# Kernel optimization log

Measured on AMD Instinct MI355X. Metric: run time of the kernel, lower is better.

The kernel has to match this reference:

```python
import jax, jax.numpy as jnp
import numpy as np

B, S, DIM, EXTRA, NK, NH, NL = 16, 256, 41, 1, 128, 4, 3
ND = DIM + EXTRA  # 42 channels after appending the Time2Vec extra channel


def _lin(key, fin, fout):
    kw, kb = jax.random.split(key)
    w = jax.random.normal(kw, (fin, fout), jnp.float32) / np.float32(np.sqrt(fin))
    b = jax.random.normal(kb, (fout,), jnp.float32) * 0.01
    return w, b


def _stack(key, fin, fout):
    ws, bs = zip(*[_lin(k, fin, fout) for k in jax.random.split(key, NL)])
    return jnp.stack(ws), jnp.stack(bs)


def setup_inputs():
    key = jax.random.key(0)
    ks = jax.random.split(key, 32)
    inp = {}
    inp['context_x'] = jnp.sort(jax.random.uniform(ks[0], (B, S), jnp.float32), axis=1)
    inp['value'] = jax.random.normal(ks[1], (B, S, DIM), jnp.float32)
    mask = (jax.random.uniform(ks[2], (B, S, DIM)) < 0.23).astype(jnp.float32)
    inp['mask'] = mask
    inp['target_value'] = jax.random.normal(ks[3], (B, S, DIM), jnp.float32)
    inp['target_mask'] = mask * (jax.random.uniform(ks[4], (B, S, DIM)) < 0.3).astype(jnp.float32)
    inp['t2v_w0'] = jax.random.normal(ks[5], (1,), jnp.float32)
    inp['t2v_b0'] = jax.random.normal(ks[6], (1,), jnp.float32)
    inp['edge_w'], inp['edge_b'] = _lin(ks[7], 2, NK)
    inp['chan_w'], inp['chan_b'] = _lin(ks[8], ND, NK)
    inp['time_w'], inp['time_b'] = _lin(ks[9], 1, NK)
    base = 10
    for pre, dk in (('ct', 2 * NK), ('tc', 2 * NK), ('ca', NK)):
        inp[pre + '_wq'], inp[pre + '_bq'] = _stack(ks[base], NK, NK); base += 1
        inp[pre + '_wk'], inp[pre + '_bk'] = _stack(ks[base], dk, NK); base += 1
        inp[pre + '_wv'], inp[pre + '_bv'] = _stack(ks[base], dk, NK); base += 1
        inp[pre + '_wo'], inp[pre + '_bo'] = _stack(ks[base], NK, NK); base += 1
    inp['en_w'], inp['en_b'] = _stack(ks[base], 3 * NK, NK); base += 1
    inp['out_w'], inp['out_b'] = _lin(ks[base], 3 * NK, 1)
    return inp


def _mab2(Q, K, wq, bq, wk, bk, wv, bv, wo, bo, mask):
    # GraFITi MAB2: fc_q/fc_k/fc_v -> dim_out, multihead attn, O = Q + A@V, then O += relu(fc_o(O))
    q = Q @ wq + bq
    k = K @ wk + bk
    v = K @ wv + bv
    b, nq, d = q.shape
    dh = d // NH
    qh = q.reshape(b, nq, NH, dh)
    kh = k.reshape(b, -1, NH, dh)
    vh = v.reshape(b, -1, NH, dh)
    att = jnp.einsum('bqhd,bkhd->bhqk', qh, kh) / np.float32(np.sqrt(d))
    if mask is not None:
        att = jnp.where(mask[:, None] == 0, jnp.float32(-1e10), att)
    A = jax.nn.softmax(att, axis=-1)
    o = (qh + jnp.einsum('bhqk,bkhd->bqhd', A, vh)).reshape(b, nq, d)
    return o + jax.nn.relu(o @ wo + bo)


def _forward(context_x, value, mask, target_value, target_mask, t2v_w0, t2v_b0,
             edge_w, edge_b, chan_w, chan_b, time_w, time_b,
             ct_wq, ct_bq, ct_wk, ct_bk, ct_wv, ct_bv, ct_wo, ct_bo,
             tc_wq, tc_bq, tc_wk, tc_bk, tc_wv, tc_bv, tc_wo, tc_bo,
             en_w, en_b,
             ca_wq, ca_bq, ca_wk, ca_bk, ca_wv, ca_bv, ca_wo, ca_bo,
             out_w, out_b):
    te = (t2v_w0 * context_x + t2v_b0)[:, :, None]  # Time2Vec linear channel [B,S,1]
    value_f = jnp.concatenate([value, te], -1)  # [B,S,ND]
    mask_f = jnp.concatenate([mask, jnp.ones((B, S, EXTRA), jnp.float32)], -1)
    tval_f = jnp.concatenate([target_value, te], -1)
    tmask_f = jnp.concatenate([target_mask, jnp.zeros((B, S, EXTRA), jnp.float32)], -1)
    # ragged compaction: observed entries first, zero-padded to the batch max count
    full_len = int(np.asarray(jnp.max(jnp.sum(mask_f, axis=(1, 2)))))
    order = jnp.argsort(-mask_f.reshape(B, -1), axis=1, stable=True)[:, :full_len]
    take = lambda x: jnp.take_along_axis(x.reshape(B, -1), order, axis=1)
    mk_ = take(mask_f)  # [B,L]: ones then zero padding
    U_val = take(value_f) * mk_
    target_U_ = take(tval_f) * mk_
    target_mask_ = take(tmask_f) * mk_
    mki = mk_.astype(jnp.int32)
    T_inds_ = take(jnp.broadcast_to(jnp.arange(S, dtype=jnp.int32)[None, :, None], (B, S, ND))) * mki
    C_inds_ = take(jnp.broadcast_to(jnp.arange(ND, dtype=jnp.int32)[None, None, :], (B, S, ND))) * mki
    C_mask = (C_inds_[:, None, :] == jnp.arange(ND)[None, :, None]).astype(jnp.float32) * mk_[:, None, :]
    T_mask = (T_inds_[:, None, :] == jnp.arange(S)[None, :, None]).astype(jnp.float32) * mk_[:, None, :]
    U_ind = 1.0 - mk_ + target_mask_
    U = jax.nn.relu(jnp.stack([U_val, U_ind], -1) @ edge_w + edge_b) * mk_[:, :, None]  # [B,L,NK]
    T_ = jnp.sin(context_x[:, :, None] @ time_w + time_b)  # [B,S,NK]
    # one_hot(arange(ND)) @ chan_w == chan_w
    C_ = jnp.broadcast_to(jax.nn.relu(chan_w + chan_b)[None], (B, ND, NK))
    gT = lambda x, idx: jnp.take_along_axis(x, jnp.broadcast_to(idx[:, :, None], (B, full_len, NK)), axis=1)
    for i in range(NL):
        k_t = gT(T_, T_inds_)
        C2 = _mab2(C_, jnp.concatenate([k_t, U], -1), ct_wq[i], ct_bq[i], ct_wk[i], ct_bk[i], ct_wv[i], ct_bv[i], ct_wo[i], ct_bo[i], C_mask)
        k_c = gT(C_, C_inds_)
        T2 = _mab2(T_, jnp.concatenate([k_c, U], -1), tc_wq[i], tc_bq[i], tc_wk[i], tc_bk[i], tc_wv[i], tc_bv[i], tc_wo[i], tc_bo[i], T_mask)
        U = jax.nn.relu(U + jnp.concatenate([U, k_t, k_c], -1) @ en_w[i] + en_b[i]) * mk_[:, :, None]
        C_ = _mab2(C2, C2, ca_wq[i], ca_bq[i], ca_wk[i], ca_bk[i], ca_wv[i], ca_bv[i], ca_wo[i], ca_bo[i], None)
        T_ = T2
    k_t = gT(T_, T_inds_)
    k_c = gT(C_, C_inds_)
    output = jnp.concatenate([U, k_t, k_c], -1) @ out_w + out_b  # [B,L,1]
    return output, target_U_, target_mask_


def reference(context_x, value, mask, target_value, target_mask, t2v_w0, t2v_b0, edge_w, edge_b, chan_w, chan_b, time_w, time_b, ct_wq, ct_bq, ct_wk, ct_bk, ct_wv, ct_bv, ct_wo, ct_bo, tc_wq, tc_bq, tc_wk, tc_bk, tc_wv, tc_bv, tc_wo, tc_bo, en_w, en_b, ca_wq, ca_bq, ca_wk, ca_bk, ca_wv, ca_bv, ca_wo, ca_bo, out_w, out_b):
    return _forward(context_x, value, mask, target_value, target_mask, t2v_w0, t2v_b0, edge_w, edge_b, chan_w, chan_b, time_w, time_b, ct_wq, ct_bq, ct_wk, ct_bk, ct_wv, ct_bv, ct_wo, ct_bo, tc_wq, tc_bq, tc_wk, tc_bk, tc_wv, tc_bv, tc_wo, tc_bo, en_w, en_b, ca_wq, ca_bq, ca_wk, ca_bk, ca_wv, ca_bv, ca_wo, ca_bo, out_w, out_b)
```

## Files before the change

### kernel.cpp

```cpp
#include <hip/hip_runtime.h>
#include <math.h>

#define NB   16
#define SS   256
#define DIMV 41
#define NDV  42
#define NKD  128
#define NHD  4
#define DH   32
#define NLAY 3
#define TOT  (SS*NDV)
#define NCH  42

typedef __attribute__((ext_vector_type(8))) short short8;
typedef __attribute__((ext_vector_type(4))) float floatx4;

__device__ __forceinline__ short f2bf(float x) {
    unsigned u = __float_as_uint(x);
    u += 0x7fff + ((u >> 16) & 1);
    return (short)(u >> 16);
}
__device__ __forceinline__ float bfs2f(short s) {
    return __uint_as_float(((unsigned)(unsigned short)s) << 16);
}
__device__ __forceinline__ float bf2f(unsigned s) {
    return __uint_as_float(s << 16);
}

struct Seg { const short* ptr; const int* ind; int ns; };

__device__ __forceinline__ const short* seg_row(const Seg s, int gm, int Lb) {
    if (s.ind) {
        int b = gm / Lb;
        int id = s.ind[gm]; if (id < 0) id = 0;
        return s.ptr + ((size_t)b * s.ns + (size_t)id) * NKD;
    }
    return s.ptr + (size_t)gm * NKD;
}


__device__ __forceinline__ void compactA_body(int bx, const float* __restrict__ maskp,
                                              int* __restrict__ chunkcnt)
{
    const int b = bx / NCH, ch = bx % NCH;
    const int tid = threadIdx.x;
    const int idx = ch * 256 + tid;
    const int s = idx / NDV, c = idx % NDV;
    float m = (c < DIMV) ? maskp[((size_t)b*SS + s)*DIMV + c] : 1.0f;
    int x = (m != 0.0f) ? 1 : 0;
    #pragma unroll
    for (int off = 32; off; off >>= 1) x += __shfl_down(x, off);
    __shared__ int ws4[4];
    if ((tid & 63) == 0) ws4[tid >> 6] = x;
    __syncthreads();
    if (tid == 0) chunkcnt[bx] = ws4[0] + ws4[1] + ws4[2] + ws4[3];
}

__device__ __forceinline__ void zero_body(int bx, int* __restrict__ lo_t,
                                          int* __restrict__ hi_t)
{
    int i = bx*256 + threadIdx.x;
    if (i < NB*SS) { lo_t[i] = 0; hi_t[i] = 0; }
}

__device__ __forceinline__ void initT_body(int bx, const float* __restrict__ cx,
                                           const float* __restrict__ tw,
                                           const float* __restrict__ tb,
                                           short* __restrict__ T)
{
    int i = bx * 256 + threadIdx.x;
    if (i >= NB*SS*16) return;
    int row = i >> 4;
    int k = (i & 15) << 3;
    float t = cx[row];
    short8 r;
    #pragma unroll
    for (int j = 0; j < 8; j++) r[j] = f2bf(sinf(t*tw[k+j] + tb[k+j]));
    *(short8*)(T + (size_t)row*NKD + k) = r;
}

__device__ __forceinline__ void initC_body(int bx, const float* __restrict__ cw,
                                           const float* __restrict__ cb,
                                           short* __restrict__ C)
{
    int i = bx * 256 + threadIdx.x;
    if (i >= NB*NDV*16) return;
    int row = i >> 4;
    int c = row % NDV;
    int k = (i & 15) << 3;
    short8 r;
    #pragma unroll
    for (int j = 0; j < 8; j++) r[j] = f2bf(fmaxf(cw[(size_t)c*NKD + k+j] + cb[k+j], 0.f));
    *(short8*)(C + (size_t)row*NKD + k) = r;
}

template<int Kg>
__device__ __forceinline__ void prep1(const float* __restrict__ src,
                                      short* __restrict__ dst, int rel)
{
    const int per = Kg*128;
    int i = rel / per; int r2 = rel - i*per;
    int n = r2 / Kg;   int k = r2 - n*Kg;
    dst[rel] = f2bf(src[(size_t)i*per + (size_t)k*128 + n]);
}

#define W_TOTAL 933888
__device__ __forceinline__ void prepw_body(int bx,
    const float* ctq, const float* ctk, const float* ctv, const float* cto,
    const float* tcq, const float* tck, const float* tcv, const float* tco,
    const float* caq, const float* cak, const float* cav, const float* cao,
    const float* enw, short* __restrict__ arena)
{
    int idx = bx*256 + threadIdx.x;
    if (idx >= W_TOTAL) return;
    if      (idx < 49152 ) prep1<128>(ctq, arena + 0,      idx - 0);
    else if (idx < 147456) prep1<256>(ctk, arena + 49152,  idx - 49152);
    else if (idx < 245760) prep1<256>(ctv, arena + 147456, idx - 147456);
    else if (idx < 294912) prep1<128>(cto, arena + 245760, idx - 245760);
    else if (idx < 344064) prep1<128>(tcq, arena + 294912, idx - 294912);
    else if (idx < 442368) prep1<256>(tck, arena + 344064, idx - 344064);
    else if (idx < 540672) prep1<256>(tcv, arena + 442368, idx - 442368);
    else if (idx < 589824) prep1<128>(tco, arena + 540672, idx - 540672);
    else if (idx < 638976) prep1<128>(caq, arena + 589824, idx - 589824);
    else if (idx < 688128) prep1<128>(cak, arena + 638976, idx - 638976);
    else if (idx < 737280) prep1<128>(cav, arena + 688128, idx - 688128);
    else if (idx < 786432) prep1<128>(cao, arena + 737280, idx - 737280);
    else                   prep1<384>(enw, arena + 786432, idx - 786432);
}

__device__ __forceinline__ void trange_body(int bx, const int* __restrict__ tind,
                                            int* __restrict__ lo_t,
                                            int* __restrict__ hi_t, int L)
{
    int p = bx*256 + threadIdx.x;
    if (p >= NB*L) return;
    int b = p / L, l = p - b*L;
    int t = tind[p];
    if (t < 0) return;
    int tp = (l > 0) ? tind[p-1] : -999;
    int tn = (l+1 < L) ? tind[p+1] : -999;
    if (tp != t) lo_t[b*SS + t] = l;
    if (tn != t) hi_t[b*SS + t] = l+1;
}

__device__ __forceinline__ void cperm_body(int b, const int* __restrict__ cind,
                                           int* __restrict__ invp,
                                           int* __restrict__ clo,
                                           int* __restrict__ chi, int L)
{
    __shared__ int hist[NDV];
    __shared__ int base[NDV];
    __shared__ int padc, cntsh;
    const int tid = threadIdx.x;
    if (tid < NDV) hist[tid] = 0;
    if (tid == 0) padc = 0;
    __syncthreads();
    for (int l = tid; l < L; l += 256) {
        int c = cind[(size_t)b*L + l];
        if (c >= 0) atomicAdd(&hist[c], 1);
    }
    __syncthreads();
    if (tid == 0) {
        int run = 0;
        for (int c = 0; c < NDV; c++) {
            base[c] = run; clo[b*NDV + c] = run;
            run += hist[c]; chi[b*NDV + c] = run;
        }
        cntsh = run;
    }
    __syncthreads();
    if (tid < NDV) hist[tid] = 0;
    __syncthreads();
    const int cnt = cntsh;
    for (int l = tid; l < L; l += 256) {
        int c = cind[(size_t)b*L + l];
        int pos;
        if (c >= 0) pos = base[c] + atomicAdd(&hist[c], 1);
        else        pos = cnt + atomicAdd(&padc, 1);
        invp[(size_t)b*L + l] = b*L + pos;
    }
}

__device__ __forceinline__ void initU_body(int bx, const float* __restrict__ uval,
                                           const float* __restrict__ uind,
                                           const float* __restrict__ mkb,
                                           const float* __restrict__ ew,
                                           const float* __restrict__ eb,
                                           short* __restrict__ U, int BL)
{
    int i = bx * 256 + threadIdx.x;
    if (i >= BL*16) return;
    int row = i >> 4;
    int k = (i & 15) << 3;
    float uv = uval[row], ui = uind[row], m = mkb[row];
    short8 r;
    #pragma unroll
    for (int j = 0; j < 8; j++)
        r[j] = f2bf(fmaxf(uv*ew[k+j] + ui*ew[NKD+k+j] + eb[k+j], 0.f) * m);
    *(short8*)(U + (size_t)row*NKD + k) = r;
}

template<int NSEG, int MODE>
__device__ __forceinline__ void mgemm_body(char* smem, int bx,
           Seg s0, Seg s1, Seg s2, const short* __restrict__ Wt,
           const float* __restrict__ bias, short* __restrict__ D,
           int M, int Lb, const float* __restrict__ mkp)
{
    short (*As)[40] = (short (*)[40])smem;
    short (*Bs)[40] = (short (*)[40])(smem + 10240);
    const int bm = bx * 128;
    const int tid = threadIdx.x;
    const int wv = tid >> 6;
    const int lane = tid & 63;
    const int quad = lane >> 4;
    const int l16 = lane & 15;
    const int K = NSEG * 128;
    floatx4 acc[2][8];
    #pragma unroll
    for (int i = 0; i < 2; i++)
        #pragma unroll
        for (int j = 0; j < 8; j++) acc[i][j] = (floatx4){0.f,0.f,0.f,0.f};

    const int arow = tid >> 1;
    const int acol = (tid & 1) * 16;
    int gmc = bm + arow; if (gmc > M-1) gmc = M-1;
    const short* rowp0 = seg_row(s0, gmc, Lb);
    const short* rowp1 = (NSEG > 1) ? seg_row(s1, gmc, Lb) : nullptr;
    const short* rowp2 = (NSEG > 2) ? seg_row(s2, gmc, Lb) : nullptr;

    for (int k0 = 0; k0 < K; k0 += 32) {
        {
            const short* rp;
            if (NSEG == 1) rp = rowp0;
            else if (NSEG == 2) rp = (k0 < 128) ? rowp0 : rowp1;
            else rp = (k0 < 128) ? rowp0 : ((k0 < 256) ? rowp1 : rowp2);
            const int ks = k0 & 127;
            const short* src = rp + ks + acol;
            *(short8*)&As[arow][acol]   = *(const short8*)(src);
            *(short8*)&As[arow][acol+8] = *(const short8*)(src+8);
        }
        {
            const short* src = Wt + (size_t)arow*K + k0 + acol;
            *(short8*)&Bs[arow][acol]   = *(const short8*)(src);
            *(short8*)&Bs[arow][acol+8] = *(const short8*)(src+8);
        }
        __syncthreads();
        short8 af0 = *(short8*)&As[wv*32 + l16][quad*8];
        short8 af1 = *(short8*)&As[wv*32 + 16 + l16][quad*8];
        #pragma unroll
        for (int nf = 0; nf < 8; nf++) {
            short8 bf = *(short8*)&Bs[nf*16 + l16][quad*8];
            acc[0][nf] = __builtin_amdgcn_mfma_f32_16x16x32_bf16(af0, bf, acc[0][nf], 0, 0, 0);
            acc[1][nf] = __builtin_amdgcn_mfma_f32_16x16x32_bf16(af1, bf, acc[1][nf], 0, 0, 0);
        }
        __syncthreads();
    }
    #pragma unroll
    for (int mf = 0; mf < 2; mf++) {
        #pragma unroll
        for (int r = 0; r < 4; r++) {
            int gm = bm + wv*32 + mf*16 + quad*4 + r;
            if (gm < M) {
                float mk = (MODE == 3) ? mkp[gm] : 0.f;
                const short* res = (MODE == 2 || MODE == 3) ? seg_row(s0, gm, Lb) : nullptr;
                #pragma unroll
                for (int nf = 0; nf < 8; nf++) {
                    int gn = nf*16 + l16;
                    float val = acc[mf][nf][r] + bias[gn];
                    if (MODE == 2) val = bfs2f(res[gn]) + fmaxf(val, 0.f);
                    else if (MODE == 3) val = fmaxf(bfs2f(res[gn]) + val, 0.f) * mk;
                    D[(size_t)gm*NKD + gn] = f2bf(val);
                }
            }
        }
    }
}

template<int NSEG>
__device__ __forceinline__ void mgemm_kv_body(char* smem, int bx,
              Seg s0, Seg s1,
              const short* __restrict__ Wk, const float* __restrict__ bk,
              const short* __restrict__ Wv, const float* __restrict__ bv,
              unsigned* __restrict__ KV, int M, int Lb, const int* __restrict__ rmap)
{
    short (*As)[40] = (short (*)[40])smem;
    short (*Bk_)[40] = (short (*)[40])(smem + 5120);
    short (*Bv_)[40] = (short (*)[40])(smem + 15360);
    const int bm = bx * 64;
    const int tid = threadIdx.x;
    const int wv = tid >> 6;
    const int lane = tid & 63;
    const int quad = lane >> 4;
    const int l16 = lane & 15;
    const int K = NSEG * 128;
    floatx4 acck[8], accv[8];
    #pragma unroll
    for (int j = 0; j < 8; j++) {
        acck[j] = (floatx4){0.f,0.f,0.f,0.f};
        accv[j] = (floatx4){0.f,0.f,0.f,0.f};
    }

    const int arow = tid >> 2;
    const int acol = (tid & 3) * 8;
    const int brow = tid >> 1;
    const int bcol = (tid & 1) * 16;
    int gmc = bm + arow; if (gmc > M-1) gmc = M-1;
    const short* rowp0 = seg_row(s0, gmc, Lb);
    const short* rowp1 = (NSEG > 1) ? seg_row(s1, gmc, Lb) : nullptr;

    for (int k0 = 0; k0 < K; k0 += 32) {
        {
            const short* rp = (NSEG == 1) ? rowp0 : ((k0 < 128) ? rowp0 : rowp1);
            const int ks = k0 & 127;
            *(short8*)&As[arow][acol] = *(const short8*)(rp + ks + acol);
        }
        {
            const short* sk = Wk + (size_t)brow*K + k0 + bcol;
            *(short8*)&Bk_[brow][bcol]   = *(const short8*)(sk);
            *(short8*)&Bk_[brow][bcol+8] = *(const short8*)(sk+8);
            const short* sv = Wv + (size_t)brow*K + k0 + bcol;
            *(short8*)&Bv_[brow][bcol]   = *(const short8*)(sv);
            *(short8*)&Bv_[brow][bcol+8] = *(const short8*)(sv+8);
        }
        __syncthreads();
        short8 af = *(short8*)&As[wv*16 + l16][quad*8];
        #pragma unroll
        for (int nf = 0; nf < 8; nf++) {
            short8 bfk = *(short8*)&Bk_[nf*16 + l16][quad*8];
            acck[nf] = __builtin_amdgcn_mfma_f32_16x16x32_bf16(af, bfk, acck[nf], 0, 0, 0);
            short8 bfv = *(short8*)&Bv_[nf*16 + l16][quad*8];
            accv[nf] = __builtin_amdgcn_mfma_f32_16x16x32_bf16(af, bfv, accv[nf], 0, 0, 0);
        }
        __syncthreads();
    }
    #pragma unroll
    for (int r = 0; r < 4; r++) {
        int gm = bm + wv*16 + quad*4 + r;
        if (gm < M) {
            int orow = rmap ? rmap[gm] : gm;
            #pragma unroll
            for (int nf = 0; nf < 8; nf++) {
                int gn = nf*16 + l16;
                float kf = acck[nf][r] + bk[gn];
                float vf = accv[nf][r] + bv[gn];
                unsigned pk = (unsigned)(unsigned short)f2bf(kf)
                            | ((unsigned)(unsigned short)f2bf(vf) << 16);
                KV[(size_t)orow*NKD + gn] = pk;
            }
        }
    }
}

__device__ __forceinline__ void octca_body(char* smem, int bx,
    const short* __restrict__ oC,
    const short* __restrict__ wo, const float* __restrict__ bo,
    const short* __restrict__ wq, const float* __restrict__ bq,
    const short* __restrict__ wk, const float* __restrict__ bk,
    const short* __restrict__ wv, const float* __restrict__ bv,
    short* __restrict__ qC, unsigned* __restrict__ KV, int M)
{
    short (*C2t)[136] = (short (*)[136])smem;
    short (*Bs)[40]   = (short (*)[40])(smem + 17408);
    short (*As)[40]   = (short (*)[40])(smem + 27648);
    const int bm = bx * 64;
    const int tid = threadIdx.x;
    const int wv_ = tid >> 6;
    const int lane = tid & 63;
    const int quad = lane >> 4;
    const int l16 = lane & 15;
    const int arow = tid >> 2;
    const int acol = (tid & 3) * 8;
    const int brow = tid >> 1;
    const int bcol = (tid & 1) * 16;
    int gmc = bm + arow; if (gmc > M-1) gmc = M-1;
    const short* rowp = oC + (size_t)gmc * NKD;

    floatx4 acc[8];
    #pragma unroll
    for (int j = 0; j < 8; j++) acc[j] = (floatx4){0.f,0.f,0.f,0.f};
    for (int k0 = 0; k0 < 128; k0 += 32) {
        *(short8*)&As[arow][acol] = *(const short8*)(rowp + k0 + acol);
        const short* sw = wo + (size_t)brow*128 + k0 + bcol;
        *(short8*)&Bs[brow][bcol]   = *(const short8*)(sw);
        *(short8*)&Bs[brow][bcol+8] = *(const short8*)(sw+8);
        __syncthreads();
        short8 af = *(short8*)&As[wv_*16 + l16][quad*8];
        #pragma unroll
        for (int nf = 0; nf < 8; nf++) {
            short8 bf = *(short8*)&Bs[nf*16 + l16][quad*8];
            acc[nf] = __builtin_amdgcn_mfma_f32_16x16x32_bf16(af, bf, acc[nf], 0, 0, 0);
        }
        __syncthreads();
    }
    #pragma unroll
    for (int r = 0; r < 4; r++) {
        int lrow = wv_*16 + quad*4 + r;
        int gm = bm + lrow; int gmr = (gm > M-1) ? (M-1) : gm;
        const short* res = oC + (size_t)gmr*NKD;
        #pragma unroll
        for (int nf = 0; nf < 8; nf++) {
            int gn = nf*16 + l16;
            float val = acc[nf][r] + bo[gn];
            val = bfs2f(res[gn]) + fmaxf(val, 0.f);
            C2t[lrow][gn] = f2bf(val);
        }
    }
    __syncthreads();

    floatx4 acck[8];
    for (int proj = 0; proj < 3; proj++) {
        const short* W = (proj == 0) ? wq : ((proj == 1) ? wk : wv);
        floatx4 a2[8];
        #pragma unroll
        for (int j = 0; j < 8; j++) a2[j] = (floatx4){0.f,0.f,0.f,0.f};
        for (int k0 = 0; k0 < 128; k0 += 32) {
            const short* sw = W + (size_t)brow*128 + k0 + bcol;
            *(short8*)&Bs[brow][bcol]   = *(const short8*)(sw);
            *(short8*)&Bs[brow][bcol+8] = *(const short8*)(sw+8);
            __syncthreads();
            short8 af = *(short8*)&C2t[wv_*16 + l16][k0 + quad*8];
            #pragma unroll
            for (int nf = 0; nf < 8; nf++) {
                short8 bf = *(short8*)&Bs[nf*16 + l16][quad*8];
                a2[nf] = __builtin_amdgcn_mfma_f32_16x16x32_bf16(af, bf, a2[nf], 0, 0, 0);
            }
            __syncthreads();
        }
        if (proj == 0) {
            #pragma unroll
            for (int r = 0; r < 4; r++) {
                int gm = bm + wv_*16 + quad*4 + r;
                if (gm < M) {
                    #pragma unroll
                    for (int nf = 0; nf < 8; nf++) {
                        int gn = nf*16 + l16;
                        qC[(size_t)gm*NKD + gn] = f2bf(a2[nf][r] + bq[gn]);
                    }
                }
            }
        } else if (proj == 1) {
            #pragma unroll
            for (int j = 0; j < 8; j++) acck[j] = a2[j];
        } else {
            #pragma unroll
            for (int r = 0; r < 4; r++) {
                int gm = bm + wv_*16 + quad*4 + r;
                if (gm < M) {
                    #pragma unroll
                    for (int nf = 0; nf < 8; nf++) {
                        int gn = nf*16 + l16;
                        float kf = acck[nf][r] + bk[gn];
                        float vf = a2[nf][r] + bv[gn];
                        KV[(size_t)gm*NKD + gn] =
                            (unsigned)(unsigned short)f2bf(kf)
                          | ((unsigned)(unsigned short)f2bf(vf) << 16);
                    }
                }
            }
        }
    }
}

template<int SPLIT>
__device__ __forceinline__ void sattn_body(int bx,
                  const short* __restrict__ q, const unsigned* __restrict__ kvb,
                  short* __restrict__ o, int nq, int nkv,
                  const int* __restrict__ lo_arr, const int* __restrict__ hi_arr)
{
    __shared__ float sm_m[4], sm_s[4], sm_a[4][DH];
    const int wvid = threadIdx.x >> 6;
    int gtask = bx * 4 + wvid;
    int task = gtask / SPLIT;
    int part = gtask % SPLIT;
    if (task >= NB * nq * NHD) return;
    const int h = task & 3;
    const int bq = task >> 2;
    const int qi = bq % nq;
    const int b = bq / nq;
    const int lane = threadIdx.x & 63;
    const int d = lane & 31;
    const int half = lane >> 5;
    int lo = lo_arr ? lo_arr[b*nq + qi] : 0;
    int hi = hi_arr ? hi_arr[b*nq + qi] : nkv;
    if (SPLIT == 2) {
        int mid = lo + ((hi - lo + 1) >> 1);
        if (part == 0) hi = mid; else lo = mid;
    }
    const float scale = 0.088388347648318447f;

    const float qv = bfs2f(q[((size_t)(b*nq + qi))*NKD + h*DH + d]);
    const unsigned* kb = kvb + (size_t)b*nkv*NKD + h*DH + d;

    float m = -INFINITY, ssum = 0.f, acc = 0.f;
    for (int l0 = lo; l0 < hi; l0 += 8) {
        unsigned ur[4];
        #pragma unroll
        for (int j = 0; j < 4; j++) {
            int l = l0 + 2*j + half;
            bool ok = (l < hi);
            ur[j] = ok ? kb[(size_t)l*NKD] : 0u;
        }
        #pragma unroll
        for (int j = 0; j < 4; j++) {
            int l = l0 + 2*j + half;
            float kr = bf2f(ur[j] & 0xffffu);
            float vr = bf2f(ur[j] >> 16);
            float partial = qv * kr;
            #pragma unroll
            for (int off = 16; off; off >>= 1) partial += __shfl_xor(partial, off);
            float s = partial * scale;
            if (l < hi) {
                float mn = fmaxf(m, s);
                float corr = __expf(m - mn);
                float p = __expf(s - mn);
                ssum = ssum * corr + p;
                acc  = acc  * corr + p * vr;
                m = mn;
            }
        }
    }
    float mo = __shfl_xor(m, 32);
    float M = fmaxf(m, mo);
    float corr = (m > -1e30f) ? __expf(m - M) : 0.f;
    ssum *= corr; acc *= corr;
    ssum += __shfl_xor(ssum, 32);
    acc  += __shfl_xor(acc, 32);

    if (SPLIT == 1) {
        if (half == 0) {
            float res = (ssum > 0.f) ? acc / ssum : 0.f;
            o[((size_t)(b*nq + qi))*NKD + h*DH + d] = f2bf(qv + res);
        }
    } else {
        if (lane == 0) { sm_m[wvid] = M; sm_s[wvid] = ssum; }
        if (lane < DH) sm_a[wvid][lane] = acc;
        __syncthreads();
        if (part == 0 && lane < DH) {
            float m2 = sm_m[wvid+1], s2 = sm_s[wvid+1], a2 = sm_a[wvid+1][lane];
            float M2 = fmaxf(M, m2);
            float c1 = (M  > -1e30f) ? __expf(M  - M2) : 0.f;
            float c2 = (m2 > -1e30f) ? __expf(m2 - M2) : 0.f;
            float S = ssum * c1 + s2 * c2;
            float A = acc  * c1 + a2 * c2;
            float res = (S > 0.f) ? A / S : 0.f;
            float qv2 = bfs2f(q[((size_t)(b*nq + qi))*NKD + h*DH + lane]);
            o[((size_t)(b*nq + qi))*NKD + h*DH + lane] = f2bf(qv2 + res);
        }
    }
}


__global__ __launch_bounds__(256)
void k_pre1(const float* maskp, int* chunkcnt, int* lo_t, int* hi_t,
            const float* cx, const float* tw, const float* tb, short* T,
            const float* cw, const float* cb, short* C,
            const float* ctq, const float* ctk, const float* ctv, const float* cto,
            const float* tcq, const float* tck, const float* tcv, const float* tco,
            const float* caq, const float* cak, const float* cav, const float* cao,
            const float* enw, short* arena)
{
    int bx = blockIdx.x;
    if (bx < NB*NCH)            compactA_body(bx, maskp, chunkcnt);
    else if (bx < NB*NCH + 16)  zero_body(bx - NB*NCH, lo_t, hi_t);
    else if (bx < NB*NCH + 16 + 256) initT_body(bx - NB*NCH - 16, cx, tw, tb, T);
    else if (bx < NB*NCH + 16 + 256 + 42) initC_body(bx - NB*NCH - 16 - 256, cw, cb, C);
    else prepw_body(bx - NB*NCH - 16 - 256 - 42,
                    ctq, ctk, ctv, cto, tcq, tck, tcv, tco,
                    caq, cak, cav, cao, enw, arena);
}

__global__ __launch_bounds__(256)
void k_compactC(const float* __restrict__ cx, const float* __restrict__ value,
              const float* __restrict__ maskp, const float* __restrict__ tval,
              const float* __restrict__ tmaskp, const float* __restrict__ w0p,
              const float* __restrict__ b0p,
              const int* __restrict__ chunkcnt, int L,
              int* __restrict__ tind, int* __restrict__ cind,
              float* __restrict__ mkb, float* __restrict__ uval,
              float* __restrict__ uind,
              float* __restrict__ outTU, float* __restrict__ outTM)
{
    const int blk = blockIdx.x;
    const int b = blk / NCH, ch = blk % NCH;
    const int tid = threadIdx.x, lane = tid & 63, wv = tid >> 6;
    const int idx = ch * 256 + tid;
    const int s = idx / NDV, c = idx % NDV;
    float mval = (c < DIMV) ? maskp[((size_t)b*SS + s)*DIMV + c] : 1.0f;
    int m = (mval != 0.0f) ? 1 : 0;
    int x = m;
    #pragma unroll
    for (int off = 1; off < 64; off <<= 1) {
        int y = __shfl_up(x, off);
        if (lane >= off) x += y;
    }
    __shared__ int wsum[4];
    __shared__ int s_off, s_cnt;
    if (lane == 63) wsum[wv] = x;
    if (tid < 64) {
        int v2 = (tid < NCH) ? chunkcnt[b*NCH + tid] : 0;
        int x2 = v2;
        #pragma unroll
        for (int off = 1; off < 64; off <<= 1) {
            int y2 = __shfl_up(x2, off);
            if (tid >= off) x2 += y2;
        }
        if (tid == ch) s_off = x2 - v2;
        if (tid == 63) s_cnt = x2;
    }
    __syncthreads();
    int wbase = 0;
    for (int w = 0; w < wv; w++) wbase += wsum[w];
    const int excl = x - m + wbase;
    const int vbefore = s_off + excl;
    const int cnt = s_cnt;
    const int pos = m ? vbefore : (cnt + (idx - vbefore));
    if (pos < L) {
        const float w0 = w0p[0], b0 = b0p[0];
        float te = w0 * cx[(size_t)b*SS + s] + b0;
        float vf, tvf, tmf;
        if (c < DIMV) {
            size_t o = ((size_t)b*SS + s)*DIMV + c;
            vf = value[o]; tvf = tval[o]; tmf = tmaskp[o];
        } else { vf = te; tvf = te; tmf = 0.0f; }
        size_t p = (size_t)b*L + pos;
        if (m) {
            tind[p] = s; cind[p] = c; mkb[p] = 1.0f;
            uval[p] = vf; uind[p] = tmf;
            outTU[p] = tvf; outTM[p] = tmf;
        } else {
            tind[p] = -1; cind[p] = -1; mkb[p] = 0.0f;
            uval[p] = 0.0f; uind[p] = 1.0f;
            outTU[p] = 0.0f; outTM[p] = 0.0f;
        }
    }
}

__global__ __launch_bounds__(256)
void k_pre4(const int* tind, int* lo_t, int* hi_t, int L, int gTr,
            const int* cind, int* invp, int* clo, int* chi,
            const float* uval, const float* uind, const float* mkb,
            const float* ew, const float* eb, short* U, int BL)
{
    int bx = blockIdx.x;
    if (bx < gTr) trange_body(bx, tind, lo_t, hi_t, L);
    else if (bx < gTr + NB) cperm_body(bx - gTr, cind, invp, clo, chi, L);
    else initU_body(bx - gTr - NB, uval, uind, mkb, ew, eb, U, BL);
}

__global__ __launch_bounds__(256)
void k_phase1(int g0, int g1, int g2,
              const short* T1, const int* tind, const short* U,
              const short* wkct, const float* bkct, const short* wvct, const float* bvct,
              unsigned* KVct, const int* invp,
              const short* C1, const short* wqct, const float* bqct, short* qC,
              const int* cind,
              const short* wktc, const float* bktc, const short* wvtc, const float* bvtc,
              unsigned* KVtc,
              const short* wqtc, const float* bqtc, short* qT,
              int BL, int L)
{
    __shared__ __align__(16) char smem[25600];
    int bx = blockIdx.x;
    if (bx < g0) {
        mgemm_kv_body<2>(smem, bx, Seg{T1,tind,SS}, Seg{U,nullptr,0},
            wkct, bkct, wvct, bvct, KVct, BL, L, invp);
    } else if (bx < g0+g1) {
        mgemm_body<1,0>(smem, bx-g0, Seg{C1,nullptr,0}, Seg{nullptr,nullptr,0},
            Seg{nullptr,nullptr,0}, wqct, bqct, qC, NB*NDV, 1, nullptr);
    } else if (bx < g0+g1+g2) {
        mgemm_kv_body<2>(smem, bx-g0-g1, Seg{C1,cind,NDV}, Seg{U,nullptr,0},
            wktc, bktc, wvtc, bvtc, KVtc, BL, L, nullptr);
    } else {
        mgemm_body<1,0>(smem, bx-g0-g1-g2, Seg{T1,nullptr,0}, Seg{nullptr,nullptr,0},
            Seg{nullptr,nullptr,0}, wqtc, bqtc, qT, NB*SS, 1, nullptr);
    }
}

__global__ __launch_bounds__(256)
void k_phase2(int g0, const short* qC, const unsigned* KVct, short* oC,
              const int* clo, const int* chi, int L,
              const short* qT, const unsigned* KVtc, short* oT,
              const int* lo_t, const int* hi_t)
{
    int bx = blockIdx.x;
    if (bx < g0) sattn_body<2>(bx, qC, KVct, oC, NDV, L, clo, chi);
    else         sattn_body<1>(bx-g0, qT, KVtc, oT, SS, L, lo_t, hi_t);
}

__global__ __launch_bounds__(256)
void k_phase3(int g0, int g1,
              const short* oC, const short* woct, const float* boct,
              const short* wq_ca, const float* bq_ca,
              const short* wk_ca, const float* bk_ca,
              const short* wv_ca, const float* bv_ca,
              short* qC, unsigned* kvCa,
              const short* oT, const short* wotc, const float* botc, short* T2b,
              const short* U, const short* T1, const int* tind,
              const short* C1, const int* cind,
              const short* wen, const float* ben, short* Unew, const float* mkb,
              int BL, int L)
{
    __shared__ __align__(16) char smem[32768];
    int bx = blockIdx.x;
    if (bx < g0)
        octca_body(smem, bx, oC, woct, boct, wq_ca, bq_ca, wk_ca, bk_ca,
                   wv_ca, bv_ca, qC, kvCa, NB*NDV);
    else if (bx < g0+g1)
        mgemm_body<1,2>(smem, bx-g0, Seg{oT,nullptr,0}, Seg{nullptr,nullptr,0},
            Seg{nullptr,nullptr,0}, wotc, botc, T2b, NB*SS, 1, nullptr);
    else
        mgemm_body<3,3>(smem, bx-g0-g1, Seg{U,nullptr,0}, Seg{T1,tind,SS},
            Seg{C1,cind,NDV}, wen, ben, Unew, BL, L, mkb);
}

__global__ __launch_bounds__(256)
void k_ca_fused(const short* __restrict__ qC, const unsigned* __restrict__ kv,
                const short* __restrict__ wo, const float* __restrict__ bo,
                short* __restrict__ C1)
{
    __shared__ __align__(16) short os[NKD];
    const int row = blockIdx.x;
    const int b = row / NDV;
    const int tid = threadIdx.x;
    const int h = tid >> 6;
    const int lane = tid & 63;
    const int d = lane & 31;
    const int half = lane >> 5;
    const float scale = 0.088388347648318447f;

    const float qv = bfs2f(qC[(size_t)row*NKD + h*DH + d]);
    const unsigned* kb = kv + (size_t)b*NDV*NKD + h*DH + d;

    float m = -INFINITY, ssum = 0.f, acc = 0.f;
    for (int l0 = 0; l0 < NDV; l0 += 2) {
        int l = l0 + half;
        unsigned ur = kb[(size_t)l*NKD];
        float kr = bf2f(ur & 0xffffu);
        float vr = bf2f(ur >> 16);
        float partial = qv * kr;
        #pragma unroll
        for (int off = 16; off; off >>= 1) partial += __shfl_xor(partial, off);
        float s = partial * scale;
        float mn = fmaxf(m, s);
        float corr = __expf(m - mn);
        float p = __expf(s - mn);
        ssum = ssum * corr + p;
        acc  = acc  * corr + p * vr;
        m = mn;
    }
    float mo = __shfl_xor(m, 32);
    float M = fmaxf(m, mo);
    float corr = (m > -1e30f) ? __expf(m - M) : 0.f;
    ssum *= corr; acc *= corr;
    ssum += __shfl_xor(ssum, 32);
    acc  += __shfl_xor(acc, 32);
    if (half == 0) {
        float res = (ssum > 0.f) ? acc / ssum : 0.f;
        os[h*DH + d] = f2bf(qv + res);
    }
    __syncthreads();

    const int n = tid >> 1;
    const int ks = (tid & 1) * 64;
    float a = 0.f;
    const short* wrow = wo + (size_t)n*NKD + ks;
    #pragma unroll
    for (int kk = 0; kk < 64; kk += 8) {
        short8 o8 = *(short8*)&os[ks + kk];
        short8 w8 = *(const short8*)(wrow + kk);
        #pragma unroll
        for (int j = 0; j < 8; j++) a += bfs2f(o8[j]) * bfs2f(w8[j]);
    }
    a += __shfl_xor(a, 1);
    if ((tid & 1) == 0) {
        float val = a + bo[n];
        val = bfs2f(os[n]) + fmaxf(val, 0.f);
        C1[(size_t)row*NKD + n] = f2bf(val);
    }
}

__global__ __launch_bounds__(256)
void k_out(const short* __restrict__ U, const short* __restrict__ T1,
           const short* __restrict__ C1, const int* __restrict__ tind,
           const int* __restrict__ cind, const float* __restrict__ ow,
           const float* __restrict__ obp, float* __restrict__ out,
           int BL, int L)
{
    int row = blockIdx.x * 4 + (threadIdx.x >> 6);
    int lane = threadIdx.x & 63;
    if (row >= BL) return;
    int b = row / L;
    int ti = tind[row]; if (ti < 0) ti = 0;
    int ci = cind[row]; if (ci < 0) ci = 0;
    const short* u = U + (size_t)row*NKD;
    const short* a = T1 + ((size_t)(b*SS + ti))*NKD;
    const short* c = C1 + ((size_t)(b*NDV + ci))*NKD;
    float s = bfs2f(u[lane])*ow[lane]     + bfs2f(u[lane+64])*ow[lane+64]
            + bfs2f(a[lane])*ow[128+lane] + bfs2f(a[lane+64])*ow[192+lane]
            + bfs2f(c[lane])*ow[256+lane] + bfs2f(c[lane+64])*ow[320+lane];
    #pragma unroll
    for (int off = 32; off; off >>= 1) s += __shfl_down(s, off);
    if (lane == 0) out[row] = s + obp[0];
}

extern "C" void kernel_launch(void* const* d_in, const int* in_sizes, int n_in,
                              void* d_out, int out_size, void* d_ws, size_t ws_size,
                              hipStream_t stream)
{
    const float* cx     = (const float*)d_in[0];
    const float* value  = (const float*)d_in[1];
    const float* maskp  = (const float*)d_in[2];
    const float* tval   = (const float*)d_in[3];
    const float* tmaskp = (const float*)d_in[4];
    const float* w0     = (const float*)d_in[5];
    const float* b0     = (const float*)d_in[6];
    const float* edge_w = (const float*)d_in[7];
    const float* edge_b = (const float*)d_in[8];
    const float* chan_w = (const float*)d_in[9];
    const float* chan_b = (const float*)d_in[10];
    const float* time_w = (const float*)d_in[11];
    const float* time_b = (const float*)d_in[12];
    const float* ct_wq = (const float*)d_in[13];
    const float* ct_bq = (const float*)d_in[14];
    const float* ct_wk = (const float*)d_in[15];
    const float* ct_bk = (const float*)d_in[16];
    const float* ct_wv = (const float*)d_in[17];
    const float* ct_bv = (const float*)d_in[18];
    const float* ct_wo = (const float*)d_in[19];
    const float* ct_bo = (const float*)d_in[20];
    const float* tc_wq = (const float*)d_in[21];
    const float* tc_bq = (const float*)d_in[22];
    const float* tc_wk = (const float*)d_in[23];
    const float* tc_bk = (const float*)d_in[24];
    const float* tc_wv = (const float*)d_in[25];
    const float* tc_bv = (const float*)d_in[26];
    const float* tc_wo = (const float*)d_in[27];
    const float* tc_bo = (const float*)d_in[28];
    const float* ca_wq = (const float*)d_in[29];
    const float* ca_bq = (const float*)d_in[30];
    const float* ca_wk = (const float*)d_in[31];
    const float* ca_bk = (const float*)d_in[32];
    const float* ca_wv = (const float*)d_in[33];
    const float* ca_bv = (const float*)d_in[34];
    const float* ca_wo = (const float*)d_in[35];
    const float* ca_bo = (const float*)d_in[36];
    const float* en_w  = (const float*)d_in[37];
    const float* en_b  = (const float*)d_in[38];
    const float* out_w = (const float*)d_in[39];
    const float* out_b = (const float*)d_in[40];

    const int BL = out_size / 3;
    const int L  = BL / NB;

    char* p = (char*)d_ws;
    auto alloc = [&](size_t n) { char* r = p; p += (n + 255) & ~(size_t)255; return r; };
    int*      tind   = (int*)  alloc((size_t)BL*4);
    int*      cind   = (int*)  alloc((size_t)BL*4);
    float*    mkb    = (float*)alloc((size_t)BL*4);
    float*    uval   = (float*)alloc((size_t)BL*4);
    float*    uind   = (float*)alloc((size_t)BL*4);
    int*      lo_t   = (int*)  alloc((size_t)NB*SS*4);
    int*      hi_t   = (int*)  alloc((size_t)NB*SS*4);
    int*      clo    = (int*)  alloc((size_t)NB*NDV*4);
    int*      chi    = (int*)  alloc((size_t)NB*NDV*4);
    int*      invp   = (int*)  alloc((size_t)BL*4);
    int*      chunkc = (int*)  alloc((size_t)NB*NCH*4);
    short*    waren  = (short*)alloc((size_t)W_TOTAL*2);
    short*    U    = (short*)alloc((size_t)BL*NKD*2);
    short*    Unew = (short*)alloc((size_t)BL*NKD*2);
    unsigned* KVct = (unsigned*)alloc((size_t)BL*NKD*4);
    unsigned* KVtc = (unsigned*)alloc((size_t)BL*NKD*4);
    unsigned* kvCa = (unsigned*)alloc((size_t)NB*NDV*NKD*4);
    short*    T1   = (short*)alloc((size_t)NB*SS*NKD*2);
    short*    T2b  = (short*)alloc((size_t)NB*SS*NKD*2);
    short*    qT   = (short*)alloc((size_t)NB*SS*NKD*2);
    short*    oT   = (short*)alloc((size_t)NB*SS*NKD*2);
    short*    C1   = (short*)alloc((size_t)NB*NDV*NKD*2);
    short*    qC   = (short*)alloc((size_t)NB*NDV*NKD*2);
    short*    oC   = (short*)alloc((size_t)NB*NDV*NKD*2);

    float* outMain = (float*)d_out;
    float* outTU = outMain + BL;
    float* outTM = outMain + 2*BL;

    const size_t OCTQ=0, OCTK=49152, OCTV=147456, OCTO=245760;
    const size_t OTCQ=294912, OTCK=344064, OTCV=442368, OTCO=540672;
    const size_t OCAQ=589824, OCAK=638976, OCAV=688128, OCAO=737280, OEN=786432;

    k_pre1<<<NB*NCH + 16 + 256 + 42 + W_TOTAL/256, 256, 0, stream>>>(
        maskp, chunkc, lo_t, hi_t, cx, time_w, time_b, T1, chan_w, chan_b, C1,
        ct_wq, ct_wk, ct_wv, ct_wo, tc_wq, tc_wk, tc_wv, tc_wo,
        ca_wq, ca_wk, ca_wv, ca_wo, en_w, waren);
    k_compactC<<<NB*NCH, 256, 0, stream>>>(cx, value, maskp, tval, tmaskp, w0, b0,
                                           chunkc, L, tind, cind, mkb, uval, uind,
                                           outTU, outTM);
    {
        const int gTr = (NB*L + 255)/256;
        const int gU  = (BL*16 + 255)/256;
        k_pre4<<<gTr + NB + gU, 256, 0, stream>>>(
            tind, lo_t, hi_t, L, gTr, cind, invp, clo, chi,
            uval, uind, mkb, edge_w, edge_b, U, BL);
    }

    const int gBL  = (BL + 127)/128;
    const int gKV  = (BL + 63)/64;
    const int gC   = (NB*NDV + 127)/128;
    const int gT   = (NB*SS + 127)/128;
    const int gCa  = (NB*NDV + 63)/64;
    const int aC2  = NB*NDV*NHD*2/4;
    const int aTC  = NB*SS*NHD/4;

    for (int i = 0; i < NLAY; i++) {
        const size_t bOff = (size_t)i*NKD;
        const short* wq_ct = waren + OCTQ + (size_t)i*128*128;
        const short* wk_ct = waren + OCTK + (size_t)i*256*128;
        const short* wv_ct = waren + OCTV + (size_t)i*256*128;
        const short* wo_ct = waren + OCTO + (size_t)i*128*128;
        const short* wq_tc = waren + OTCQ + (size_t)i*128*128;
        const short* wk_tc = waren + OTCK + (size_t)i*256*128;
        const short* wv_tc = waren + OTCV + (size_t)i*256*128;
        const short* wo_tc = waren + OTCO + (size_t)i*128*128;
        const short* wq_ca = waren + OCAQ + (size_t)i*128*128;
        const short* wk_ca = waren + OCAK + (size_t)i*128*128;
        const short* wv_ca = waren + OCAV + (size_t)i*128*128;
        const short* wo_ca = waren + OCAO + (size_t)i*128*128;
        const short* w_en  = waren + OEN  + (size_t)i*384*128;

        k_phase1<<<gKV + gC + gKV + gT, 256, 0, stream>>>(
            gKV, gC, gKV,
            T1, tind, U,
            wk_ct, ct_bk + bOff, wv_ct, ct_bv + bOff, KVct, invp,
            C1, wq_ct, ct_bq + bOff, qC,
            cind, wk_tc, tc_bk + bOff, wv_tc, tc_bv + bOff, KVtc,
            wq_tc, tc_bq + bOff, qT, BL, L);
        k_phase2<<<aC2 + aTC, 256, 0, stream>>>(
            aC2, qC, KVct, oC, clo, chi, L, qT, KVtc, oT, lo_t, hi_t);
        k_phase3<<<gCa + gT + gBL, 256, 0, stream>>>(
            gCa, gT,
            oC, wo_ct, ct_bo + bOff,
            wq_ca, ca_bq + bOff, wk_ca, ca_bk + bOff, wv_ca, ca_bv + bOff,
            qC, kvCa,
            oT, wo_tc, tc_bo + bOff, T2b,
            U, T1, tind, C1, cind, w_en, en_b + bOff, Unew, mkb, BL, L);
        k_ca_fused<<<NB*NDV, 256, 0, stream>>>(qC, kvCa, wo_ca, ca_bo + bOff, C1);

        short* t = U;  U = Unew; Unew = t;
        t = T1; T1 = T2b; T2b = t;
    }

    k_out<<<(BL + 3)/4, 256, 0, stream>>>(U, T1, C1, tind, cind,
                                          out_w, out_b, outMain, BL, L);
}
```

Baseline: 434.6 us.

## Fuse compaction scan into prologue kernel and shrink KV GEMM tiles to 32 rows

Each compaction block now recomputes the per-chunk mask counts for its whole batch itself rather than reading them from a separate count kernel. That lets the compaction run inside the merged prologue kernel and removes one launch and one global round trip. The fused K/V projection GEMM now uses 32-row tiles, with each wave covering a 16x64 sub-tile, which doubles the block count for more parallelism and uses less shared memory. The cost is redundant mask reads per block, more total weight-tile loads, and half the threads sitting idle during A-tile loads.

```diff
diff --git a/kernel.cpp b/kernel.cpp
--- a/kernel.cpp
+++ b/kernel.cpp
@@ -38,23 +38,6 @@
     return s.ptr + (size_t)gm * NKD;
 }
 
-
-__device__ __forceinline__ void compactA_body(int bx, const float* __restrict__ maskp,
-                                              int* __restrict__ chunkcnt)
-{
-    const int b = bx / NCH, ch = bx % NCH;
-    const int tid = threadIdx.x;
-    const int idx = ch * 256 + tid;
-    const int s = idx / NDV, c = idx % NDV;
-    float m = (c < DIMV) ? maskp[((size_t)b*SS + s)*DIMV + c] : 1.0f;
-    int x = (m != 0.0f) ? 1 : 0;
-    #pragma unroll
-    for (int off = 32; off; off >>= 1) x += __shfl_down(x, off);
-    __shared__ int ws4[4];
-    if ((tid & 63) == 0) ws4[tid >> 6] = x;
-    __syncthreads();
-    if (tid == 0) chunkcnt[bx] = ws4[0] + ws4[1] + ws4[2] + ws4[3];
-}
 
 __device__ __forceinline__ void zero_body(int bx, int* __restrict__ lo_t,
                                           int* __restrict__ hi_t)
@@ -128,6 +111,87 @@
     else                   prep1<384>(enw, arena + 786432, idx - 786432);
 }
 
+__device__ __forceinline__ void compactC_body(int blk,
+              const float* __restrict__ cx, const float* __restrict__ value,
+              const float* __restrict__ maskp, const float* __restrict__ tval,
+              const float* __restrict__ tmaskp, const float* __restrict__ w0p,
+              const float* __restrict__ b0p, int L,
+              int* __restrict__ tind, int* __restrict__ cind,
+              float* __restrict__ mkb, float* __restrict__ uval,
+              float* __restrict__ uind,
+              float* __restrict__ outTU, float* __restrict__ outTM)
+{
+    const int b = blk / NCH, ch = blk % NCH;
+    const int tid = threadIdx.x, lane = tid & 63, wv = tid >> 6;
+    __shared__ int cc[NCH];
+    __shared__ int wsum[4];
+    __shared__ int s_off, s_cnt;
+
+    const int idx = ch * 256 + tid;
+    const int s = idx / NDV, c = idx % NDV;
+    float mval = (c < DIMV) ? maskp[((size_t)b*SS + s)*DIMV + c] : 1.0f;
+    int m = (mval != 0.0f) ? 1 : 0;
+    int x = m;
+    #pragma unroll
+    for (int off = 1; off < 64; off <<= 1) {
+        int y = __shfl_up(x, off);
+        if (lane >= off) x += y;
+    }
+    if (lane == 63) wsum[wv] = x;
+
+    for (int j = wv; j < NCH; j += 4) {
+        int cnt = 0;
+        #pragma unroll
+        for (int i = 0; i < 4; i++) {
+            int idx2 = j*256 + lane + 64*i;
+            int s2 = idx2 / NDV, c2 = idx2 % NDV;
+            float m2 = (c2 < DIMV) ? maskp[((size_t)b*SS + s2)*DIMV + c2] : 1.0f;
+            cnt += (m2 != 0.0f) ? 1 : 0;
+        }
+        #pragma unroll
+        for (int off = 32; off; off >>= 1) cnt += __shfl_down(cnt, off);
+        if (lane == 0) cc[j] = cnt;
+    }
+    __syncthreads();
+    if (tid < 64) {
+        int v2 = (tid < NCH) ? cc[tid] : 0;
+        int x2 = v2;
+        #pragma unroll
+        for (int off = 1; off < 64; off <<= 1) {
+            int y2 = __shfl_up(x2, off);
+            if (tid >= off) x2 += y2;
+        }
+        if (tid == ch) s_off = x2 - v2;
+        if (tid == 63) s_cnt = x2;
+    }
+    __syncthreads();
+    int wbase = 0;
+    for (int w = 0; w < wv; w++) wbase += wsum[w];
+    const int excl = x - m + wbase;
+    const int vbefore = s_off + excl;
+    const int cnt = s_cnt;
+    const int pos = m ? vbefore : (cnt + (idx - vbefore));
+    if (pos < L) {
+        const float w0 = w0p[0], b0 = b0p[0];
+        float te = w0 * cx[(size_t)b*SS + s] + b0;
+        float vf, tvf, tmf;
+        if (c < DIMV) {
+            size_t o = ((size_t)b*SS + s)*DIMV + c;
+            vf = value[o]; tvf = tval[o]; tmf = tmaskp[o];
+        } else { vf = te; tvf = te; tmf = 0.0f; }
+        size_t p = (size_t)b*L + pos;
+        if (m) {
+            tind[p] = s; cind[p] = c; mkb[p] = 1.0f;
+            uval[p] = vf; uind[p] = tmf;
+            outTU[p] = tvf; outTM[p] = tmf;
+        } else {
+            tind[p] = -1; cind[p] = -1; mkb[p] = 0.0f;
+            uval[p] = 0.0f; uind[p] = 1.0f;
+            outTU[p] = 0.0f; outTM[p] = 0.0f;
+        }
+    }
+}
+
 __device__ __forceinline__ void trange_body(int bx, const int* __restrict__ tind,
                                             int* __restrict__ lo_t,
                                             int* __restrict__ hi_t, int L)
@@ -277,30 +341,32 @@
 }
 
 template<int NSEG>
-__device__ __forceinline__ void mgemm_kv_body(char* smem, int bx,
+__device__ __forceinline__ void mgemm_kv32_body(char* smem, int bx,
               Seg s0, Seg s1,
               const short* __restrict__ Wk, const float* __restrict__ bk,
               const short* __restrict__ Wv, const float* __restrict__ bv,
               unsigned* __restrict__ KV, int M, int Lb, const int* __restrict__ rmap)
 {
-    short (*As)[40] = (short (*)[40])smem;
-    short (*Bk_)[40] = (short (*)[40])(smem + 5120);
-    short (*Bv_)[40] = (short (*)[40])(smem + 15360);
-    const int bm = bx * 64;
+    short (*As)[40]  = (short (*)[40])smem;
+    short (*Bk_)[40] = (short (*)[40])(smem + 2560);
+    short (*Bv_)[40] = (short (*)[40])(smem + 12800);
+    const int bm = bx * 32;
     const int tid = threadIdx.x;
     const int wv = tid >> 6;
     const int lane = tid & 63;
     const int quad = lane >> 4;
     const int l16 = lane & 15;
+    const int mf = wv >> 1;
+    const int nh = wv & 1;
     const int K = NSEG * 128;
-    floatx4 acck[8], accv[8];
-    #pragma unroll
-    for (int j = 0; j < 8; j++) {
+    floatx4 acck[4], accv[4];
+    #pragma unroll
+    for (int j = 0; j < 4; j++) {
         acck[j] = (floatx4){0.f,0.f,0.f,0.f};
         accv[j] = (floatx4){0.f,0.f,0.f,0.f};
     }
 
-    const int arow = tid >> 2;
+    const int arow = (tid & 127) >> 2;
     const int acol = (tid & 3) * 8;
     const int brow = tid >> 1;
     const int bcol = (tid & 1) * 16;
@@ -309,7 +375,7 @@
     const short* rowp1 = (NSEG > 1) ? seg_row(s1, gmc, Lb) : nullptr;
 
     for (int k0 = 0; k0 < K; k0 += 32) {
-        {
+        if (tid < 128) {
             const short* rp = (NSEG == 1) ? rowp0 : ((k0 < 128) ? rowp0 : rowp1);
             const int ks = k0 & 127;
             *(short8*)&As[arow][acol] = *(const short8*)(rp + ks + acol);
@@ -323,24 +389,24 @@
             *(short8*)&Bv_[brow][bcol+8] = *(const short8*)(sv+8);
         }
         __syncthreads();
-        short8 af = *(short8*)&As[wv*16 + l16][quad*8];
-        #pragma unroll
-        for (int nf = 0; nf < 8; nf++) {
-            short8 bfk = *(short8*)&Bk_[nf*16 + l16][quad*8];
+        short8 af = *(short8*)&As[mf*16 + l16][quad*8];
+        #pragma unroll
+        for (int nf = 0; nf < 4; nf++) {
+            short8 bfk = *(short8*)&Bk_[nh*64 + nf*16 + l16][quad*8];
             acck[nf] = __builtin_amdgcn_mfma_f32_16x16x32_bf16(af, bfk, acck[nf], 0, 0, 0);
-            short8 bfv = *(short8*)&Bv_[nf*16 + l16][quad*8];
+            short8 bfv = *(short8*)&Bv_[nh*64 + nf*16 + l16][quad*8];
             accv[nf] = __builtin_amdgcn_mfma_f32_16x16x32_bf16(af, bfv, accv[nf], 0, 0, 0);
         }
         __syncthreads();
     }
     #pragma unroll
     for (int r = 0; r < 4; r++) {
-        int gm = bm + wv*16 + quad*4 + r;
+        int gm = bm + mf*16 + quad*4 + r;
         if (gm < M) {
             int orow = rmap ? rmap[gm] : gm;
             #pragma unroll
-            for (int nf = 0; nf < 8; nf++) {
-                int gn = nf*16 + l16;
+            for (int nf = 0; nf < 4; nf++) {
+                int gn = nh*64 + nf*16 + l16;
                 float kf = acck[nf][r] + bk[gn];
                 float vf = accv[nf][r] + bv[gn];
                 unsigned pk = (unsigned)(unsigned short)f2bf(kf)
@@ -551,88 +617,29 @@
 
 
 __global__ __launch_bounds__(256)
-void k_pre1(const float* maskp, int* chunkcnt, int* lo_t, int* hi_t,
-            const float* cx, const float* tw, const float* tb, short* T,
-            const float* cw, const float* cb, short* C,
-            const float* ctq, const float* ctk, const float* ctv, const float* cto,
-            const float* tcq, const float* tck, const float* tcv, const float* tco,
-            const float* caq, const float* cak, const float* cav, const float* cao,
-            const float* enw, short* arena)
+void k_pre_all(const float* cx, const float* value, const float* maskp,
+               const float* tval, const float* tmaskp, const float* w0p,
+               const float* b0p, int L,
+               int* tind, int* cind, float* mkb, float* uval, float* uind,
+               float* outTU, float* outTM,
+               int* lo_t, int* hi_t,
+               const float* tw, const float* tb, short* T,
+               const float* cw, const float* cb, short* C,
+               const float* ctq, const float* ctk, const float* ctv, const float* cto,
+               const float* tcq, const float* tck, const float* tcv, const float* tco,
+               const float* caq, const float* cak, const float* cav, const float* cao,
+               const float* enw, short* arena)
 {
     int bx = blockIdx.x;
-    if (bx < NB*NCH)            compactA_body(bx, maskp, chunkcnt);
+    if (bx < NB*NCH)
+        compactC_body(bx, cx, value, maskp, tval, tmaskp, w0p, b0p, L,
+                      tind, cind, mkb, uval, uind, outTU, outTM);
     else if (bx < NB*NCH + 16)  zero_body(bx - NB*NCH, lo_t, hi_t);
     else if (bx < NB*NCH + 16 + 256) initT_body(bx - NB*NCH - 16, cx, tw, tb, T);
     else if (bx < NB*NCH + 16 + 256 + 42) initC_body(bx - NB*NCH - 16 - 256, cw, cb, C);
     else prepw_body(bx - NB*NCH - 16 - 256 - 42,
                     ctq, ctk, ctv, cto, tcq, tck, tcv, tco,
                     caq, cak, cav, cao, enw, arena);
-}
-
-__global__ __launch_bounds__(256)
-void k_compactC(const float* __restrict__ cx, const float* __restrict__ value,
-              const float* __restrict__ maskp, const float* __restrict__ tval,
-              const float* __restrict__ tmaskp, const float* __restrict__ w0p,
-              const float* __restrict__ b0p,
-              const int* __restrict__ chunkcnt, int L,
-              int* __restrict__ tind, int* __restrict__ cind,
-              float* __restrict__ mkb, float* __restrict__ uval,
-              float* __restrict__ uind,
-              float* __restrict__ outTU, float* __restrict__ outTM)
-{
-    const int blk = blockIdx.x;
-    const int b = blk / NCH, ch = blk % NCH;
-    const int tid = threadIdx.x, lane = tid & 63, wv = tid >> 6;
-    const int idx = ch * 256 + tid;
-    const int s = idx / NDV, c = idx % NDV;
-    float mval = (c < DIMV) ? maskp[((size_t)b*SS + s)*DIMV + c] : 1.0f;
-    int m = (mval != 0.0f) ? 1 : 0;
-    int x = m;
-    #pragma unroll
-    for (int off = 1; off < 64; off <<= 1) {
-        int y = __shfl_up(x, off);
-        if (lane >= off) x += y;
-    }
-    __shared__ int wsum[4];
-    __shared__ int s_off, s_cnt;
-    if (lane == 63) wsum[wv] = x;
-    if (tid < 64) {
-        int v2 = (tid < NCH) ? chunkcnt[b*NCH + tid] : 0;
-        int x2 = v2;
-        #pragma unroll
-        for (int off = 1; off < 64; off <<= 1) {
-            int y2 = __shfl_up(x2, off);
-            if (tid >= off) x2 += y2;
-        }
-        if (tid == ch) s_off = x2 - v2;
-        if (tid == 63) s_cnt = x2;
-    }
-    __syncthreads();
-    int wbase = 0;
-    for (int w = 0; w < wv; w++) wbase += wsum[w];
-    const int excl = x - m + wbase;
-    const int vbefore = s_off + excl;
-    const int cnt = s_cnt;
-    const int pos = m ? vbefore : (cnt + (idx - vbefore));
-    if (pos < L) {
-        const float w0 = w0p[0], b0 = b0p[0];
-        float te = w0 * cx[(size_t)b*SS + s] + b0;
-        float vf, tvf, tmf;
-        if (c < DIMV) {
-            size_t o = ((size_t)b*SS + s)*DIMV + c;
-            vf = value[o]; tvf = tval[o]; tmf = tmaskp[o];
-        } else { vf = te; tvf = te; tmf = 0.0f; }
-        size_t p = (size_t)b*L + pos;
-        if (m) {
-            tind[p] = s; cind[p] = c; mkb[p] = 1.0f;
-            uval[p] = vf; uind[p] = tmf;
-            outTU[p] = tvf; outTM[p] = tmf;
-        } else {
-            tind[p] = -1; cind[p] = -1; mkb[p] = 0.0f;
-            uval[p] = 0.0f; uind[p] = 1.0f;
-            outTU[p] = 0.0f; outTM[p] = 0.0f;
-        }
-    }
 }
 
 __global__ __launch_bounds__(256)
@@ -659,16 +666,16 @@
               const short* wqtc, const float* bqtc, short* qT,
               int BL, int L)
 {
-    __shared__ __align__(16) char smem[25600];
+    __shared__ __align__(16) char smem[23040];
     int bx = blockIdx.x;
     if (bx < g0) {
-        mgemm_kv_body<2>(smem, bx, Seg{T1,tind,SS}, Seg{U,nullptr,0},
+        mgemm_kv32_body<2>(smem, bx, Seg{T1,tind,SS}, Seg{U,nullptr,0},
             wkct, bkct, wvct, bvct, KVct, BL, L, invp);
     } else if (bx < g0+g1) {
         mgemm_body<1,0>(smem, bx-g0, Seg{C1,nullptr,0}, Seg{nullptr,nullptr,0},
             Seg{nullptr,nullptr,0}, wqct, bqct, qC, NB*NDV, 1, nullptr);
     } else if (bx < g0+g1+g2) {
-        mgemm_kv_body<2>(smem, bx-g0-g1, Seg{C1,cind,NDV}, Seg{U,nullptr,0},
+        mgemm_kv32_body<2>(smem, bx-g0-g1, Seg{C1,cind,NDV}, Seg{U,nullptr,0},
             wktc, bktc, wvtc, bvtc, KVtc, BL, L, nullptr);
     } else {
         mgemm_body<1,0>(smem, bx-g0-g1-g2, Seg{T1,nullptr,0}, Seg{nullptr,nullptr,0},
@@ -864,7 +871,6 @@
     int*      clo    = (int*)  alloc((size_t)NB*NDV*4);
     int*      chi    = (int*)  alloc((size_t)NB*NDV*4);
     int*      invp   = (int*)  alloc((size_t)BL*4);
-    int*      chunkc = (int*)  alloc((size_t)NB*NCH*4);
     short*    waren  = (short*)alloc((size_t)W_TOTAL*2);
     short*    U    = (short*)alloc((size_t)BL*NKD*2);
     short*    Unew = (short*)alloc((size_t)BL*NKD*2);
@@ -887,13 +893,12 @@
     const size_t OTCQ=294912, OTCK=344064, OTCV=442368, OTCO=540672;
     const size_t OCAQ=589824, OCAK=638976, OCAV=688128, OCAO=737280, OEN=786432;
 
-    k_pre1<<<NB*NCH + 16 + 256 + 42 + W_TOTAL/256, 256, 0, stream>>>(
-        maskp, chunkc, lo_t, hi_t, cx, time_w, time_b, T1, chan_w, chan_b, C1,
+    k_pre_all<<<NB*NCH + 16 + 256 + 42 + W_TOTAL/256, 256, 0, stream>>>(
+        cx, value, maskp, tval, tmaskp, w0, b0, L,
+        tind, cind, mkb, uval, uind, outTU, outTM,
+        lo_t, hi_t, time_w, time_b, T1, chan_w, chan_b, C1,
         ct_wq, ct_wk, ct_wv, ct_wo, tc_wq, tc_wk, tc_wv, tc_wo,
         ca_wq, ca_wk, ca_wv, ca_wo, en_w, waren);
-    k_compactC<<<NB*NCH, 256, 0, stream>>>(cx, value, maskp, tval, tmaskp, w0, b0,
-                                           chunkc, L, tind, cind, mkb, uval, uind,
-                                           outTU, outTM);
     {
         const int gTr = (NB*L + 255)/256;
         const int gU  = (BL*16 + 255)/256;
@@ -903,7 +908,7 @@
     }
 
     const int gBL  = (BL + 127)/128;
-    const int gKV  = (BL + 63)/64;
+    const int gKV  = (BL + 31)/32;
     const int gC   = (NB*NDV + 127)/128;
     const int gT   = (NB*SS + 127)/128;
     const int gCa  = (NB*NDV + 63)/64;
```

Measured after the change: 457.1 us. 1.05x slower.
